# Kernel optimization log

Measured on AMD Instinct MI355X. Metric: run time of the kernel, lower is better.

## Reference

```python
import jax, jax.numpy as jnp
import numpy as np

B, L, D, H = 4, 1024, 1024, 16
HD = D // H            # head dim 64
MAXP = 1024            # max_position_embeddings
NADJ = 2               # teacher layers mapped to this student layer


def setup_inputs() -> dict:
    key = jax.random.key(0)
    ks = jax.random.split(key, 6)
    return {
        "hidden_states": jax.random.normal(ks[0], (B, L, D), jnp.float32),
        "attention_mask": jnp.zeros((B, 1, 1, L), jnp.float32),
        "teacher_w": jax.random.normal(ks[1], (3, NADJ, D, D), jnp.float32) * 0.02,
        "wl_w": jax.random.normal(ks[2], (3, NADJ), jnp.float32),
        "scale_w": jnp.ones((3, D, D), jnp.float32),
        "shift_w": jnp.zeros((3, D, D), jnp.float32),
        "teacher_b": jax.random.normal(ks[3], (3, NADJ, D), jnp.float32) * 0.02,
        "wl_b": jax.random.normal(ks[4], (3, NADJ), jnp.float32),
        "scale_b": jnp.ones((3, D), jnp.float32),
        "shift_b": jnp.zeros((3, D), jnp.float32),
        "dist_emb": jax.random.normal(ks[5], (2 * MAXP - 1, HD), jnp.float32) * 0.02,
    }


def reference(hidden_states, attention_mask, teacher_w, wl_w, scale_w, shift_w,
              teacher_b, wl_b, scale_b, shift_b, dist_emb):
    # Teacher-distilled weight/bias generation (WeightGenerator/BiasGenerator):
    # student = tanh(mode-0 contraction of teacher subset with W_l) * W + B
    w = jnp.tanh(jnp.einsum('pl,ploi->poi', wl_w, teacher_w)) * scale_w + shift_w  # [3,out,in]
    b = jnp.tanh(jnp.einsum('pl,plo->po', wl_b, teacher_b)) * scale_b + shift_b    # [3,out]

    def proj(i):
        y = jnp.einsum('bld,od->blo', hidden_states, w[i]) + b[i]
        return y.reshape(B, L, H, HD).transpose(0, 2, 1, 3)  # [B,H,L,HD]

    q, k, v = proj(0), proj(1), proj(2)

    scores = jnp.einsum('bhld,bhrd->bhlr', q, k)  # [B,H,L,L]

    # relative_key_query positional bias
    dist = jnp.arange(L)[:, None] - jnp.arange(L)[None, :] + (MAXP - 1)  # [L,L]
    pe = dist_emb[dist]                                                  # [L,L,HD]
    scores = scores \
        + jnp.einsum('bhld,lrd->bhlr', q, pe) \
        + jnp.einsum('bhrd,lrd->bhlr', k, pe)

    scores = scores / np.sqrt(HD).astype(np.float32) + attention_mask
    probs = jax.nn.softmax(scores, axis=-1)  # dropout p=0.0 (eval)

    ctx = jnp.einsum('bhlr,bhrd->bhld', probs, v)
    return ctx.transpose(0, 2, 1, 3).reshape(B, L, D)
```

## Files before the change

### kernel.cpp

```cpp
#include <hip/hip_runtime.h>
#include <hip/hip_bf16.h>
#include <math.h>

#define D_  1024
#define L_  1024
#define B_  4
#define H_  16
#define HD_ 64

typedef __attribute__((ext_vector_type(4))) short short4_t;
typedef __attribute__((ext_vector_type(8))) short short8_t;
typedef __attribute__((ext_vector_type(4))) float f4;
typedef unsigned short u16;

__device__ __forceinline__ f4 MF(short8_t a, short8_t b, f4 c) {
  return __builtin_amdgcn_mfma_f32_16x16x32_bf16(a, b, c, 0, 0, 0);
}
__device__ __forceinline__ unsigned fbits(float x) { return __builtin_bit_cast(unsigned, x); }
__device__ __forceinline__ float bf2f(unsigned short u) {
  return __builtin_bit_cast(float, (unsigned)u << 16);
}
__device__ __forceinline__ unsigned pack2hi(float x, float y) {
  return (fbits(x) >> 16) | (fbits(y) & 0xFFFF0000u);
}
__device__ __forceinline__ float bfres(float x) {
  return x - __builtin_bit_cast(float, fbits(x) & 0xFFFF0000u);
}
__device__ __forceinline__ float ftanh(float x) {
  float t = __expf(2.f * x);
  return (t - 1.f) / (t + 1.f);
}
__device__ __forceinline__ void gload16(const void* g, void* l) {
  __builtin_amdgcn_global_load_lds(
      (const __attribute__((address_space(1))) unsigned*)g,
      (__attribute__((address_space(3))) unsigned*)l, 16, 0, 0);
}
__device__ __forceinline__ short8_t ldsfragP(const char* base, int row, int ci) {
  return *(const short8_t*)(base + row * 128 + ((ci ^ (row & 7)) << 4));
}
__device__ __forceinline__ int perm32(int c) {
  return (c & ~31) | (((c >> 2) & 3) << 3) | (((c >> 4) & 1) << 2);
}

__global__ __launch_bounds__(256) void wgen_kernel(
    const float* __restrict__ tw, const float* __restrict__ wl,
    const float* __restrict__ sc, const float* __restrict__ sh,
    u16* __restrict__ whi, u16* __restrict__ wlo) {
  size_t i4 = (size_t)blockIdx.x * 256 + threadIdx.x;
  size_t e = i4 * 4;
  int p = (int)(e >> 20);
  size_t rem = e & 0xFFFFFu;
  float a0 = wl[p * 2 + 0], a1 = wl[p * 2 + 1];
  float4 t0 = *(const float4*)&tw[((size_t)(p * 2 + 0) << 20) + rem];
  float4 t1 = *(const float4*)&tw[((size_t)(p * 2 + 1) << 20) + rem];
  float4 s4 = *(const float4*)&sc[e];
  float4 h4 = *(const float4*)&sh[e];
  float4 o;
  o.x = ftanh(a0 * t0.x + a1 * t1.x) * s4.x + h4.x;
  o.y = ftanh(a0 * t0.y + a1 * t1.y) * s4.y + h4.y;
  o.z = ftanh(a0 * t0.z + a1 * t1.z) * s4.z + h4.z;
  o.w = ftanh(a0 * t0.w + a1 * t1.w) * s4.w + h4.w;
  const size_t off = (e & ~(size_t)31) + perm32((int)(e & 31));
  uint2 hi; hi.x = pack2hi(o.x, o.y); hi.y = pack2hi(o.z, o.w);
  *(uint2*)&whi[off] = hi;
  uint2 lo; lo.x = pack2hi(bfres(o.x), bfres(o.y)); lo.y = pack2hi(bfres(o.z), bfres(o.w));
  *(uint2*)&wlo[off] = lo;
}

__global__ __launch_bounds__(256) void hscvt_kernel(
    const float* __restrict__ hs,
    u16* __restrict__ hhi, u16* __restrict__ hlo) {
  size_t i4 = (size_t)blockIdx.x * 256 + threadIdx.x;
  size_t e = i4 * 4;
  float4 v = *(const float4*)&hs[e];
  const size_t off = (e & ~(size_t)31) + perm32((int)(e & 31));
  uint2 hi; hi.x = pack2hi(v.x, v.y); hi.y = pack2hi(v.z, v.w);
  *(uint2*)&hhi[off] = hi;
  uint2 lo; lo.x = pack2hi(bfres(v.x), bfres(v.y)); lo.y = pack2hi(bfres(v.z), bfres(v.w));
  *(uint2*)&hlo[off] = lo;
}

__global__ __launch_bounds__(256) void bgen_kernel(
    const float* __restrict__ tb, const float* __restrict__ wl,
    const float* __restrict__ sc, const float* __restrict__ sh,
    float* __restrict__ b_out) {
  int i = blockIdx.x * 256 + threadIdx.x;
  int p = i >> 10;
  int o = i & 1023;
  float v = ftanh(wl[p * 2 + 0] * tb[(p * 2 + 0) * D_ + o] +
                  wl[p * 2 + 1] * tb[(p * 2 + 1) * D_ + o]);
  b_out[i] = v * sc[i] + sh[i];
}

__global__ __launch_bounds__(256) void ecvt_kernel(
    const float* __restrict__ emb, u16* __restrict__ embh) {
  int i4 = blockIdx.x * 256 + threadIdx.x;
  if (i4 >= 32752) return;
  int e = i4 * 4;
  float4 v = *(const float4*)&emb[e];
  uint2 h2; h2.x = pack2hi(v.x, v.y); h2.y = pack2hi(v.z, v.w);
  int pe = (e & ~31) | perm32(e & 31);
  *(uint2*)&embh[pe] = h2;
}

__global__ __launch_bounds__(256) void proj_mfma_kernel(
    const u16* __restrict__ Ahp, const u16* __restrict__ Alp,
    const u16* __restrict__ Bhp, const u16* __restrict__ Blp,
    const float* __restrict__ bias,
    u16* __restrict__ Qhi, u16* __restrict__ Qlo,
    u16* __restrict__ Khi, u16* __restrict__ Klo,
    u16* __restrict__ Vthi, u16* __restrict__ Vtlo) {
  __shared__ u16 Ah[128][32], Al[128][32], Bh[128][32], Bl[128][32];
  const int tid  = threadIdx.x;
  const int lane = tid & 63;
  const int wv   = tid >> 6;
  const int wm   = wv >> 1, wn = wv & 1;
  const int l15  = lane & 15, g = lane >> 4;

  const int bid = (blockIdx.x & 7) * 96 + (blockIdx.x >> 3);
  const int mt = bid & 31, nt = bid >> 5;
  const int m0 = mt * 128, n0 = nt * 128;

  f4 acc[4][4];
#pragma unroll
  for (int i = 0; i < 4; ++i)
#pragma unroll
    for (int j = 0; j < 4; ++j) acc[i][j] = f4{0.f, 0.f, 0.f, 0.f};

  const int srow = lane >> 2;
  const int sck  = (lane & 3) * 8;

#pragma unroll 1
  for (int k0 = 0; k0 < D_; k0 += 32) {
#pragma unroll
    for (int s = 0; s < 8; ++s) {
      const int q = wv * 8 + s;
      const int mat   = q >> 4;
      const int plane = (q >> 3) & 1;
      const int rowg  = q & 7;
      const u16* base = mat ? (plane ? Alp : Ahp) : (plane ? Blp : Bhp);
      const int  rb   = mat ? m0 : n0;
      const u16* src = base + (size_t)(rb + rowg * 16 + srow) * 1024 + k0 + sck;
      u16* dst = (mat ? (plane ? &Al[0][0] : &Ah[0][0])
                      : (plane ? &Bl[0][0] : &Bh[0][0])) + rowg * 512;
      gload16(src, dst);
    }
    __syncthreads();

    short8_t ah[4], al[4], bh[4], bl[4];
#pragma unroll
    for (int i = 0; i < 4; ++i) {
      ah[i] = *(const short8_t*)&Ah[wm * 64 + i * 16 + l15][g * 8];
      al[i] = *(const short8_t*)&Al[wm * 64 + i * 16 + l15][g * 8];
      bh[i] = *(const short8_t*)&Bh[wn * 64 + i * 16 + l15][g * 8];
      bl[i] = *(const short8_t*)&Bl[wn * 64 + i * 16 + l15][g * 8];
    }
#pragma unroll
    for (int mi = 0; mi < 4; ++mi)
#pragma unroll
      for (int ni = 0; ni < 4; ++ni) {
        acc[mi][ni] = MF(ah[mi], bh[ni], acc[mi][ni]);
        acc[mi][ni] = MF(ah[mi], bl[ni], acc[mi][ni]);
        acc[mi][ni] = MF(al[mi], bh[ni], acc[mi][ni]);
      }
    __syncthreads();
  }

  const int p = n0 >> 10;
  const int h0 = (n0 >> 6) & 15;
  const int nbase = n0 + wn * 64;
  float bnv[4];
#pragma unroll
  for (int ni = 0; ni < 4; ++ni) bnv[ni] = bias[nbase + ni * 16 + l15];
  float* T = (float*)&Ah[0][0];

#pragma unroll
  for (int mi = 0; mi < 4; ++mi) {
    __syncthreads();
#pragma unroll
    for (int ni = 0; ni < 4; ++ni)
#pragma unroll
      for (int r = 0; r < 4; ++r)
        T[(wm * 16 + 4 * g + r) * 132 + wn * 64 + ni * 16 + l15] =
            acc[mi][ni][r] + bnv[ni];
    __syncthreads();

    if (p < 2) {
      u16* PH = p ? Khi : Qhi;
      u16* PL = p ? Klo : Qlo;
      const int lr = tid >> 3;
      const int m = m0 + (lr >> 4) * 64 + mi * 16 + (lr & 15);
      const int bb = m >> 10, l = m & 1023;
#pragma unroll
      for (int c = 0; c < 4; ++c) {
        const int col = 4 * (tid & 7) + 32 * c;
        const int pc = perm32(col & 63) | (col & 64);
        const int hd = pc & 63, hl = col >> 6;
        float4 v = *(const float4*)&T[lr * 132 + col];
        uint2 hi; hi.x = pack2hi(v.x, v.y); hi.y = pack2hi(v.z, v.w);
        uint2 lo; lo.x = pack2hi(bfres(v.x), bfres(v.y)); lo.y = pack2hi(bfres(v.z), bfres(v.w));
        const size_t ad = ((size_t)(bb * 16 + h0 + hl) << 16) + (size_t)l * 64 + hd;
        *(uint2*)&PH[ad] = hi;
        *(uint2*)&PL[ad] = lo;
      }
    } else {
      const int col = (tid >> 3) & 31;
#pragma unroll
      for (int c = 0; c < 4; ++c) {
        const int cc = col + 32 * c;
        const int hd = cc & 63, hl = cc >> 6;
        const int mq = tid & 7;
        const int lr0 = 4 * mq;
        float vv[4];
#pragma unroll
        for (int k = 0; k < 4; ++k) vv[k] = T[(lr0 + k) * 132 + cc];
        const int m = m0 + (lr0 >> 4) * 64 + mi * 16 + (lr0 & 15);
        const int bb = m >> 10, l = m & 1023;
        const int pl = (l & ~31) | perm32(l & 31);
        uint2 hi; hi.x = pack2hi(vv[0], vv[1]); hi.y = pack2hi(vv[2], vv[3]);
        uint2 lo; lo.x = pack2hi(bfres(vv[0]), bfres(vv[1]));
        lo.y = pack2hi(bfres(vv[2]), bfres(vv[3]));
        const size_t ad = ((size_t)(bb * 16 + h0 + hl) << 16) + (size_t)hd * 1024 + pl;
        *(uint2*)&Vthi[ad] = hi;
        *(uint2*)&Vtlo[ad] = lo;
      }
    }
  }
}

#define KD_OFF 0
#define VD_OFF 32768
#define ER_OFF 49152
#define UB_OFF 81920
#define WB_OFF 115712
#define SM4_SIZE 149504

__global__ __launch_bounds__(512, 2) void attn7_kernel(
    const u16* __restrict__ Qhi, const u16* __restrict__ Qlo,
    const u16* __restrict__ Khi, const u16* __restrict__ Klo,
    const u16* __restrict__ Vthi, const u16* __restrict__ Vtlo,
    const u16* __restrict__ embh, const float* __restrict__ mask,
    float* __restrict__ out) {
  __shared__ __align__(16) char sm[SM4_SIZE];
  char* ERb = sm + ER_OFF;

  const int tid  = threadIdx.x;
  const int lane = tid & 63;
  const int wv   = tid >> 6;
  const int t    = wv >> 2;
  const int lh   = (wv >> 1) & 1;
  const int rh   = wv & 1;
  const int l15  = lane & 15;
  const int g    = lane >> 4;
  const int rsub = lane >> 3;
  const int scol = ((lane & 7) ^ (lane >> 3)) << 3;

  const int bid = (blockIdx.x & 7) * 64 + (blockIdx.x >> 3);
  const int lp = bid & 7, h = (bid >> 3) & 15, b = bid >> 7;
  const int l0 = lp * 128;
  const size_t bhoff = (size_t)(b * 16 + h) << 16;
  const float* maskp = mask + b * L_;

  u16* UBt = (u16*)(sm + UB_OFF) + t * 8448;
  u16* WBt = (u16*)(sm + WB_OFF) + t * 8448;

#pragma unroll
  for (int s = 0; s < 4; ++s) {
    const int idx = wv * 4 + s;
    const int plane = idx >> 4, rowg = idx & 15;
    const u16* src = (plane ? Qlo : Qhi) + bhoff +
                     (size_t)(l0 + rowg * 8 + rsub) * 64 + scol;
    gload16(src, ERb + (plane * 16 + rowg) * 1024);
  }
  __syncthreads();

  short8_t qfh[2][2], qfl[2][2];
#pragma unroll
  for (int nb = 0; nb < 2; ++nb)
#pragma unroll
    for (int kc = 0; kc < 2; ++kc) {
      const int row = 64 * t + 32 * lh + 16 * nb + l15;
      qfh[nb][kc] = ldsfragP(ERb,         row, 4 * kc + g);
      qfl[nb][kc] = ldsfragP(ERb + 16384, row, 4 * kc + g);
    }
  __syncthreads();

  const int pl0 = (wv * 2 + 0) >> 3, rg0 = (wv * 2 + 0) & 7;
  const int pl1 = (wv * 2 + 1) >> 3, rg1 = (wv * 2 + 1) & 7;
  const u16* kb0 = (pl0 ? Klo : Khi) + bhoff + (size_t)(rg0 * 8 + rsub) * 64 + scol;
  const u16* kb1 = (pl1 ? Klo : Khi) + bhoff + (size_t)(rg1 * 8 + rsub) * 64 + scol;
  const u16* vp0 = (pl0 ? Vtlo : Vthi) + bhoff + (size_t)(rg0 * 8 + rsub) * 1024 + scol;
  const u16* vp1 = (pl1 ? Vtlo : Vthi) + bhoff + (size_t)(rg1 * 8 + rsub) * 1024 + scol;
  const u16* ep  = embh + (size_t)(l0 + 896 + wv * 8 + rsub) * 64 + scol;
  const u16* kp0 = kb0 + 4096;
  const u16* kp1 = kb1 + 4096;
  char* const kdst0 = sm + KD_OFF + pl0 * 8192 + rg0 * 1024;
  char* const kdst1 = sm + KD_OFF + pl1 * 8192 + rg1 * 1024;
  char* const vdst0 = sm + VD_OFF + pl0 * 8192 + rg0 * 1024;
  char* const vdst1 = sm + VD_OFF + pl1 * 8192 + rg1 * 1024;

  {
    gload16(kb0, kdst0);
    gload16(kb1, kdst1);
    const int dmin0 = l0 + 960;
#pragma unroll
    for (int s = 0; s < 3; ++s) {
      const int grp = wv * 3 + s;
      const int slot = (dmin0 + grp * 8) & 255;
      gload16(embh + (size_t)(dmin0 + grp * 8 + rsub) * 64 + scol,
              ERb + slot * 128);
    }
  }

  f4 o_acc[4][2];
#pragma unroll
  for (int i = 0; i < 4; ++i)
#pragma unroll
    for (int j = 0; j < 2; ++j) o_acc[i][j] = f4{0.f, 0.f, 0.f, 0.f};
  float mrun[2] = {-3e38f, -3e38f};
  float lsum[2] = {0.f, 0.f};

#pragma unroll 2
  for (int rt = 0; rt < 16; ++rt) {
    const int r0 = rt * 64;
    const int cur = rt & 1;
    const int dmin = l0 - r0 + 960;

    __syncthreads();

    if (rt < 15) {
      char* kdn = sm + KD_OFF + (cur ^ 1) * 16384;
      gload16(kp0, kdn + pl0 * 8192 + rg0 * 1024);
      gload16(kp1, kdn + pl1 * 8192 + rg1 * 1024);
      kp0 += 4096; kp1 += 4096;
      const int slot = (dmin - 64 + wv * 8) & 255;
      gload16(ep, ERb + slot * 128);
      ep -= 4096;
    }
    gload16(vp0, vdst0);
    gload16(vp1, vdst1);
    vp0 += 64; vp1 += 64;

    float4 mk[2];
#pragma unroll
    for (int mb = 0; mb < 2; ++mb)
      mk[mb] = *(const float4*)&maskp[r0 + 32 * rh + 16 * mb + 4 * g];

    const char* kdc_h = sm + KD_OFF + cur * 16384;
    const char* kdc_l = kdc_h + 8192;

    f4 sacc[2][2];
#pragma unroll
    for (int i = 0; i < 2; ++i)
#pragma unroll
      for (int j = 0; j < 2; ++j) sacc[i][j] = f4{0.f, 0.f, 0.f, 0.f};
    short8_t khf[2][2];
    __builtin_amdgcn_s_setprio(1);
#pragma unroll
    for (int mb = 0; mb < 2; ++mb)
#pragma unroll
      for (int kc = 0; kc < 2; ++kc) {
        const int row = 32 * rh + 16 * mb + l15;
        short8_t ka = ldsfragP(kdc_h, row, 4 * kc + g);
        short8_t kl = ldsfragP(kdc_l, row, 4 * kc + g);
        khf[mb][kc] = ka;
#pragma unroll
        for (int nb = 0; nb < 2; ++nb) {
          sacc[mb][nb] = MF(ka, qfh[nb][kc], sacc[mb][nb]);
          sacc[mb][nb] = MF(ka, qfl[nb][kc], sacc[mb][nb]);
          sacc[mb][nb] = MF(kl, qfh[nb][kc], sacc[mb][nb]);
        }
      }
    __builtin_amdgcn_s_setprio(0);

#pragma unroll
    for (int s = 0; s < 3; ++s) {
      const int dblk = 16 * (2 * lh + 3 * rh + s);
      const int erow = (dmin + 64 * t + dblk + l15) & 255;
      const short8_t eb0 = ldsfragP(ERb, erow, g);
      const short8_t eb1 = ldsfragP(ERb, erow, 4 + g);
      f4 au0 = f4{0.f, 0.f, 0.f, 0.f}, au1 = f4{0.f, 0.f, 0.f, 0.f};
      au0 = MF(eb0, qfh[0][0], au0); au0 = MF(eb1, qfh[0][1], au0);
      au1 = MF(eb0, qfh[1][0], au1); au1 = MF(eb1, qfh[1][1], au1);
#pragma unroll
      for (int nb = 0; nb < 2; ++nb) {
        const f4 au = nb ? au1 : au0;
        uint2 w2; w2.x = pack2hi(au[0], au[1]); w2.y = pack2hi(au[2], au[3]);
        *(uint2*)&UBt[(32 * lh + 16 * nb + l15) * 132 + dblk + 4 * g] = w2;
      }
    }

#pragma unroll
    for (int s = 0; s < 3; ++s) {
      const int dblk = 16 * ((2 - 2 * rh) + 3 * lh + s);
      const int erow = (dmin + 64 * t + dblk + l15) & 255;
      const short8_t eb0 = ldsfragP(ERb, erow, g);
      const short8_t eb1 = ldsfragP(ERb, erow, 4 + g);
      f4 aw0 = f4{0.f, 0.f, 0.f, 0.f}, aw1 = f4{0.f, 0.f, 0.f, 0.f};
      aw0 = MF(eb0, khf[0][0], aw0); aw0 = MF(eb1, khf[0][1], aw0);
      aw1 = MF(eb0, khf[1][0], aw1); aw1 = MF(eb1, khf[1][1], aw1);
#pragma unroll
      for (int mb = 0; mb < 2; ++mb) {
        const f4 aw = mb ? aw1 : aw0;
        uint2 w2; w2.x = pack2hi(aw[0], aw[1]); w2.y = pack2hi(aw[2], aw[3]);
        *(uint2*)&WBt[(32 * rh + 16 * mb + l15) * 132 + dblk + 4 * g] = w2;
      }
    }
    __syncthreads();

    float pbuf[2][2][4];
#pragma unroll
    for (int nb = 0; nb < 2; ++nb) {
      const int lA = 32 * lh + 16 * nb + l15;
      float sv[2][4];
      float ml = -3e38f;
#pragma unroll
      for (int mb = 0; mb < 2; ++mb) {
        const int rr = 32 * rh + 16 * mb + 4 * g;
        const int dbase = lA + 63 - rr;
        const float mka[4] = {mk[mb].x, mk[mb].y, mk[mb].z, mk[mb].w};
#pragma unroll
        for (int j = 0; j < 4; ++j) {
          const float uu = bf2f(UBt[lA * 132 + dbase - j]);
          const float ww = bf2f(WBt[(rr + j) * 132 + dbase - j]);
          float s = (sacc[mb][nb][j] + uu + ww) * 0.125f + mka[j];
          sv[mb][j] = s;
          ml = fmaxf(ml, s);
        }
      }
      ml = fmaxf(ml, __shfl_xor(ml, 16));
      ml = fmaxf(ml, __shfl_xor(ml, 32));
      const bool nore = __all(ml <= mrun[nb]);
      const float mn = nore ? mrun[nb] : fmaxf(mrun[nb], ml);
      float ps = 0.f;
#pragma unroll
      for (int mb = 0; mb < 2; ++mb)
#pragma unroll
        for (int j = 0; j < 4; ++j) {
          const float pv = __expf(sv[mb][j] - mn);
          pbuf[nb][mb][j] = pv;
          ps += pv;
        }
      ps += __shfl_xor(ps, 16);
      ps += __shfl_xor(ps, 32);
      if (nore) {
        lsum[nb] += ps;
      } else {
        const float rs = __expf(mrun[nb] - mn);
        lsum[nb] = lsum[nb] * rs + ps;
        mrun[nb] = mn;
#pragma unroll
        for (int mbd = 0; mbd < 4; ++mbd) {
          o_acc[mbd][nb][0] *= rs; o_acc[mbd][nb][1] *= rs;
          o_acc[mbd][nb][2] *= rs; o_acc[mbd][nb][3] *= rs;
        }
      }
    }

    short8_t pf[2], pl_[2];
#pragma unroll
    for (int nb = 0; nb < 2; ++nb) {
      union { unsigned u[4]; short8_t v; } uh, ul;
      uh.u[0] = pack2hi(pbuf[nb][0][0], pbuf[nb][0][1]);
      uh.u[1] = pack2hi(pbuf[nb][0][2], pbuf[nb][0][3]);
      uh.u[2] = pack2hi(pbuf[nb][1][0], pbuf[nb][1][1]);
      uh.u[3] = pack2hi(pbuf[nb][1][2], pbuf[nb][1][3]);
      pf[nb] = uh.v;
      ul.u[0] = pack2hi(bfres(pbuf[nb][0][0]), bfres(pbuf[nb][0][1]));
      ul.u[1] = pack2hi(bfres(pbuf[nb][0][2]), bfres(pbuf[nb][0][3]));
      ul.u[2] = pack2hi(bfres(pbuf[nb][1][0]), bfres(pbuf[nb][1][1]));
      ul.u[3] = pack2hi(bfres(pbuf[nb][1][2]), bfres(pbuf[nb][1][3]));
      pl_[nb] = ul.v;
    }
    const char* vdc_h = sm + VD_OFF;
    const char* vdc_l = vdc_h + 8192;
    __builtin_amdgcn_s_setprio(1);
#pragma unroll
    for (int mbd = 0; mbd < 4; ++mbd) {
      short8_t vh = ldsfragP(vdc_h, 16 * mbd + l15, 4 * rh + g);
      short8_t vl = ldsfragP(vdc_l, 16 * mbd + l15, 4 * rh + g);
#pragma unroll
      for (int nb = 0; nb < 2; ++nb) {
        o_acc[mbd][nb] = MF(vh, pf[nb], o_acc[mbd][nb]);
        o_acc[mbd][nb] = MF(vh, pl_[nb], o_acc[mbd][nb]);
        o_acc[mbd][nb] = MF(vl, pf[nb], o_acc[mbd][nb]);
      }
    }
    __builtin_amdgcn_s_setprio(0);
  }

  __syncthreads();
  float* mbuf = (float*)ERb;
  float* obuf = (float*)(sm + UB_OFF);
  if (g == 0) {
#pragma unroll
    for (int nb = 0; nb < 2; ++nb) {
      mbuf[((wv * 2 + nb) * 16 + l15) * 2 + 0] = mrun[nb];
      mbuf[((wv * 2 + nb) * 16 + l15) * 2 + 1] = lsum[nb];
    }
  }
  __syncthreads();
  const int pw = wv ^ 1;
  float alpha[2], ltot[2];
#pragma unroll
  for (int nb = 0; nb < 2; ++nb) {
    float m2 = mbuf[((pw * 2 + nb) * 16 + l15) * 2 + 0];
    float s2 = mbuf[((pw * 2 + nb) * 16 + l15) * 2 + 1];
    float M = fmaxf(mrun[nb], m2);
    alpha[nb] = __expf(mrun[nb] - M);
    ltot[nb] = lsum[nb] * alpha[nb] + s2 * __expf(m2 - M);
  }
  const int pair = wv >> 1;
  if (rh == 1) {
#pragma unroll
    for (int mbd = 0; mbd < 4; ++mbd)
#pragma unroll
      for (int nb = 0; nb < 2; ++nb)
#pragma unroll
        for (int j = 0; j < 4; ++j)
          obuf[(pair * 64 + 16 * mbd + 4 * g + j) * 32 + 16 * nb + l15] =
              o_acc[mbd][nb][j] * alpha[nb];
  }
  __syncthreads();
  if (rh == 0) {
#pragma unroll
    for (int mbd = 0; mbd < 4; ++mbd)
#pragma unroll
      for (int nb = 0; nb < 2; ++nb) {
        const int lgl = l0 + 64 * t + 32 * lh + 16 * nb + l15;
        const float inv = 1.f / ltot[nb];
        float tmp[4];
#pragma unroll
        for (int j = 0; j < 4; ++j)
          tmp[j] = (o_acc[mbd][nb][j] * alpha[nb] +
                    obuf[(pair * 64 + 16 * mbd + 4 * g + j) * 32 + 16 * nb + l15]) * inv;
        float4 ov; ov.x = tmp[0]; ov.y = tmp[1]; ov.z = tmp[2]; ov.w = tmp[3];
        *(float4*)&out[(size_t)(b * L_ + lgl) * D_ + h * HD_ + 16 * mbd + 4 * g] = ov;
      }
  }
}

extern "C" void kernel_launch(void* const* d_in, const int* in_sizes, int n_in,
                              void* d_out, int out_size, void* d_ws, size_t ws_size,
                              hipStream_t stream) {
  const float* hs   = (const float*)d_in[0];
  const float* mask = (const float*)d_in[1];
  const float* tw   = (const float*)d_in[2];
  const float* wlw  = (const float*)d_in[3];
  const float* scw  = (const float*)d_in[4];
  const float* shw  = (const float*)d_in[5];
  const float* tb   = (const float*)d_in[6];
  const float* wlb  = (const float*)d_in[7];
  const float* scb  = (const float*)d_in[8];
  const float* shb  = (const float*)d_in[9];
  const float* emb  = (const float*)d_in[10];
  float* out = (float*)d_out;

  char* W = (char*)d_ws;
  float* b_s = (float*)W;
  u16* whi  = (u16*)(W + 12288);
  u16* wlo  = whi + 3145728;
  u16* embh = wlo + 3145728;
  u16* Qhi  = embh + 131072;
  u16* Qlo  = Qhi + 4194304;
  u16* Khi  = Qlo + 4194304;
  u16* Klo  = Khi + 4194304;
  u16* Vthi = Klo + 4194304;
  u16* Vtlo = Vthi + 4194304;
  u16* hhi  = Vtlo + 4194304;
  u16* hlo  = hhi + 4194304;

  hipLaunchKernelGGL(wgen_kernel, dim3(3072), dim3(256), 0, stream,
                     tw, wlw, scw, shw, whi, wlo);
  hipLaunchKernelGGL(hscvt_kernel, dim3(4096), dim3(256), 0, stream,
                     hs, hhi, hlo);
  hipLaunchKernelGGL(bgen_kernel, dim3(12), dim3(256), 0, stream,
                     tb, wlb, scb, shb, b_s);
  hipLaunchKernelGGL(ecvt_kernel, dim3(128), dim3(256), 0, stream, emb, embh);
  hipLaunchKernelGGL(proj_mfma_kernel, dim3(768), dim3(256), 0, stream,
                     hhi, hlo, whi, wlo, b_s, Qhi, Qlo, Khi, Klo, Vthi, Vtlo);
  hipLaunchKernelGGL(attn7_kernel, dim3(512), dim3(512), 0, stream,
                     Qhi, Qlo, Khi, Klo, Vthi, Vtlo, embh, mask, out);
}
```

Before: 251.1 us.

## Fuse prep kernels into one launch and double-buffer projection GEMM loads

The four elementwise preparation kernels (weight generation, hidden-state split, embedding convert, bias generation) are merged into a single launch whose block ranges dispatch to each task. This removes three kernel launches and the gaps between them. The projection GEMM now double-buffers its LDS tiles: it prefetches the next k-slice while computing the current one, needs one barrier per iteration instead of two, and raises wave priority around the MFMA block. In exchange, LDS use doubles and a launch-bounds hint of 2 blocks per CU is added, which may constrain registers.

After: 231.1 us. 8.0% less time.

```diff
diff --git a/kernel.cpp b/kernel.cpp
--- a/kernel.cpp
+++ b/kernel.cpp
@@ -42,75 +42,73 @@
   return (c & ~31) | (((c >> 2) & 3) << 3) | (((c >> 4) & 1) << 2);
 }
 
-__global__ __launch_bounds__(256) void wgen_kernel(
-    const float* __restrict__ tw, const float* __restrict__ wl,
-    const float* __restrict__ sc, const float* __restrict__ sh,
-    u16* __restrict__ whi, u16* __restrict__ wlo) {
-  size_t i4 = (size_t)blockIdx.x * 256 + threadIdx.x;
-  size_t e = i4 * 4;
-  int p = (int)(e >> 20);
-  size_t rem = e & 0xFFFFFu;
-  float a0 = wl[p * 2 + 0], a1 = wl[p * 2 + 1];
-  float4 t0 = *(const float4*)&tw[((size_t)(p * 2 + 0) << 20) + rem];
-  float4 t1 = *(const float4*)&tw[((size_t)(p * 2 + 1) << 20) + rem];
-  float4 s4 = *(const float4*)&sc[e];
-  float4 h4 = *(const float4*)&sh[e];
-  float4 o;
-  o.x = ftanh(a0 * t0.x + a1 * t1.x) * s4.x + h4.x;
-  o.y = ftanh(a0 * t0.y + a1 * t1.y) * s4.y + h4.y;
-  o.z = ftanh(a0 * t0.z + a1 * t1.z) * s4.z + h4.z;
-  o.w = ftanh(a0 * t0.w + a1 * t1.w) * s4.w + h4.w;
-  const size_t off = (e & ~(size_t)31) + perm32((int)(e & 31));
-  uint2 hi; hi.x = pack2hi(o.x, o.y); hi.y = pack2hi(o.z, o.w);
-  *(uint2*)&whi[off] = hi;
-  uint2 lo; lo.x = pack2hi(bfres(o.x), bfres(o.y)); lo.y = pack2hi(bfres(o.z), bfres(o.w));
-  *(uint2*)&wlo[off] = lo;
-}
-
-__global__ __launch_bounds__(256) void hscvt_kernel(
+__global__ __launch_bounds__(256) void prep_kernel(
+    const float* __restrict__ tw, const float* __restrict__ wlw,
+    const float* __restrict__ scw, const float* __restrict__ shw,
     const float* __restrict__ hs,
-    u16* __restrict__ hhi, u16* __restrict__ hlo) {
-  size_t i4 = (size_t)blockIdx.x * 256 + threadIdx.x;
-  size_t e = i4 * 4;
-  float4 v = *(const float4*)&hs[e];
-  const size_t off = (e & ~(size_t)31) + perm32((int)(e & 31));
-  uint2 hi; hi.x = pack2hi(v.x, v.y); hi.y = pack2hi(v.z, v.w);
-  *(uint2*)&hhi[off] = hi;
-  uint2 lo; lo.x = pack2hi(bfres(v.x), bfres(v.y)); lo.y = pack2hi(bfres(v.z), bfres(v.w));
-  *(uint2*)&hlo[off] = lo;
-}
-
-__global__ __launch_bounds__(256) void bgen_kernel(
-    const float* __restrict__ tb, const float* __restrict__ wl,
-    const float* __restrict__ sc, const float* __restrict__ sh,
-    float* __restrict__ b_out) {
-  int i = blockIdx.x * 256 + threadIdx.x;
-  int p = i >> 10;
-  int o = i & 1023;
-  float v = ftanh(wl[p * 2 + 0] * tb[(p * 2 + 0) * D_ + o] +
-                  wl[p * 2 + 1] * tb[(p * 2 + 1) * D_ + o]);
-  b_out[i] = v * sc[i] + sh[i];
-}
-
-__global__ __launch_bounds__(256) void ecvt_kernel(
-    const float* __restrict__ emb, u16* __restrict__ embh) {
-  int i4 = blockIdx.x * 256 + threadIdx.x;
-  if (i4 >= 32752) return;
-  int e = i4 * 4;
-  float4 v = *(const float4*)&emb[e];
-  uint2 h2; h2.x = pack2hi(v.x, v.y); h2.y = pack2hi(v.z, v.w);
-  int pe = (e & ~31) | perm32(e & 31);
-  *(uint2*)&embh[pe] = h2;
-}
-
-__global__ __launch_bounds__(256) void proj_mfma_kernel(
+    const float* __restrict__ tb, const float* __restrict__ wlb,
+    const float* __restrict__ scb, const float* __restrict__ shb,
+    const float* __restrict__ emb,
+    u16* __restrict__ whi, u16* __restrict__ wlo,
+    u16* __restrict__ hhi, u16* __restrict__ hlo,
+    u16* __restrict__ embh, float* __restrict__ b_s) {
+  const int blk = blockIdx.x;
+  const int tid = threadIdx.x;
+  if (blk < 3072) {
+    size_t i4 = (size_t)blk * 256 + tid;
+    size_t e = i4 * 4;
+    int p = (int)(e >> 20);
+    size_t rem = e & 0xFFFFFu;
+    float a0 = wlw[p * 2 + 0], a1 = wlw[p * 2 + 1];
+    float4 t0 = *(const float4*)&tw[((size_t)(p * 2 + 0) << 20) + rem];
+    float4 t1 = *(const float4*)&tw[((size_t)(p * 2 + 1) << 20) + rem];
+    float4 s4 = *(const float4*)&scw[e];
+    float4 h4 = *(const float4*)&shw[e];
+    float4 o;
+    o.x = ftanh(a0 * t0.x + a1 * t1.x) * s4.x + h4.x;
+    o.y = ftanh(a0 * t0.y + a1 * t1.y) * s4.y + h4.y;
+    o.z = ftanh(a0 * t0.z + a1 * t1.z) * s4.z + h4.z;
+    o.w = ftanh(a0 * t0.w + a1 * t1.w) * s4.w + h4.w;
+    const size_t off = (e & ~(size_t)31) + perm32((int)(e & 31));
+    uint2 hi; hi.x = pack2hi(o.x, o.y); hi.y = pack2hi(o.z, o.w);
+    *(uint2*)&whi[off] = hi;
+    uint2 lo; lo.x = pack2hi(bfres(o.x), bfres(o.y)); lo.y = pack2hi(bfres(o.z), bfres(o.w));
+    *(uint2*)&wlo[off] = lo;
+  } else if (blk < 7168) {
+    size_t i4 = (size_t)(blk - 3072) * 256 + tid;
+    size_t e = i4 * 4;
+    float4 v = *(const float4*)&hs[e];
+    const size_t off = (e & ~(size_t)31) + perm32((int)(e & 31));
+    uint2 hi; hi.x = pack2hi(v.x, v.y); hi.y = pack2hi(v.z, v.w);
+    *(uint2*)&hhi[off] = hi;
+    uint2 lo; lo.x = pack2hi(bfres(v.x), bfres(v.y)); lo.y = pack2hi(bfres(v.z), bfres(v.w));
+    *(uint2*)&hlo[off] = lo;
+  } else if (blk < 7296) {
+    int i4 = (blk - 7168) * 256 + tid;
+    if (i4 >= 32752) return;
+    int e = i4 * 4;
+    float4 v = *(const float4*)&emb[e];
+    uint2 h2; h2.x = pack2hi(v.x, v.y); h2.y = pack2hi(v.z, v.w);
+    int pe = (e & ~31) | perm32(e & 31);
+    *(uint2*)&embh[pe] = h2;
+  } else {
+    int i = (blk - 7296) * 256 + tid;
+    int p = i >> 10;
+    int o = i & 1023;
+    float v = ftanh(wlb[p * 2 + 0] * tb[(p * 2 + 0) * D_ + o] +
+                    wlb[p * 2 + 1] * tb[(p * 2 + 1) * D_ + o]);
+    b_s[i] = v * scb[i] + shb[i];
+  }
+}
+
+__global__ __launch_bounds__(256, 2) void proj_mfma_kernel(
     const u16* __restrict__ Ahp, const u16* __restrict__ Alp,
     const u16* __restrict__ Bhp, const u16* __restrict__ Blp,
     const float* __restrict__ bias,
     u16* __restrict__ Qhi, u16* __restrict__ Qlo,
     u16* __restrict__ Khi, u16* __restrict__ Klo,
     u16* __restrict__ Vthi, u16* __restrict__ Vtlo) {
-  __shared__ u16 Ah[128][32], Al[128][32], Bh[128][32], Bl[128][32];
+  __shared__ u16 SB[2][4][128][32];
   const int tid  = threadIdx.x;
   const int lane = tid & 63;
   const int wv   = tid >> 6;
@@ -130,31 +128,45 @@
   const int srow = lane >> 2;
   const int sck  = (lane & 3) * 8;
 
-#pragma unroll 1
-  for (int k0 = 0; k0 < D_; k0 += 32) {
-#pragma unroll
-    for (int s = 0; s < 8; ++s) {
-      const int q = wv * 8 + s;
-      const int mat   = q >> 4;
-      const int plane = (q >> 3) & 1;
-      const int rowg  = q & 7;
-      const u16* base = mat ? (plane ? Alp : Ahp) : (plane ? Blp : Bhp);
-      const int  rb   = mat ? m0 : n0;
-      const u16* src = base + (size_t)(rb + rowg * 16 + srow) * 1024 + k0 + sck;
-      u16* dst = (mat ? (plane ? &Al[0][0] : &Ah[0][0])
-                      : (plane ? &Bl[0][0] : &Bh[0][0])) + rowg * 512;
-      gload16(src, dst);
-    }
+  const u16* sbase[8];
+  u16* sdst[8];
+#pragma unroll
+  for (int s = 0; s < 8; ++s) {
+    const int q = wv * 8 + s;
+    const int mat   = q >> 4;
+    const int plane = (q >> 3) & 1;
+    const int rowg  = q & 7;
+    const u16* base = mat ? (plane ? Alp : Ahp) : (plane ? Blp : Bhp);
+    const int  rb   = mat ? m0 : n0;
+    sbase[s] = base + (size_t)(rb + rowg * 16 + srow) * 1024 + sck;
+    sdst[s]  = &SB[0][(mat ^ 1) * 2 + plane][rowg * 16][0];
+  }
+
+#pragma unroll
+  for (int s = 0; s < 8; ++s) gload16(sbase[s], sdst[s]);
+
+#pragma unroll 2
+  for (int kt = 0; kt < 32; ++kt) {
+    const int cur = kt & 1;
     __syncthreads();
 
+    if (kt < 31) {
+      const int k1 = (kt + 1) * 32;
+      const int bo = (cur ^ 1) * 16384;
+#pragma unroll
+      for (int s = 0; s < 8; ++s) gload16(sbase[s] + k1, sdst[s] + bo);
+    }
+
+    const u16 (*SBc)[128][32] = SB[cur];
     short8_t ah[4], al[4], bh[4], bl[4];
 #pragma unroll
     for (int i = 0; i < 4; ++i) {
-      ah[i] = *(const short8_t*)&Ah[wm * 64 + i * 16 + l15][g * 8];
-      al[i] = *(const short8_t*)&Al[wm * 64 + i * 16 + l15][g * 8];
-      bh[i] = *(const short8_t*)&Bh[wn * 64 + i * 16 + l15][g * 8];
-      bl[i] = *(const short8_t*)&Bl[wn * 64 + i * 16 + l15][g * 8];
-    }
+      ah[i] = *(const short8_t*)&SBc[0][wm * 64 + i * 16 + l15][g * 8];
+      al[i] = *(const short8_t*)&SBc[1][wm * 64 + i * 16 + l15][g * 8];
+      bh[i] = *(const short8_t*)&SBc[2][wn * 64 + i * 16 + l15][g * 8];
+      bl[i] = *(const short8_t*)&SBc[3][wn * 64 + i * 16 + l15][g * 8];
+    }
+    __builtin_amdgcn_s_setprio(1);
 #pragma unroll
     for (int mi = 0; mi < 4; ++mi)
 #pragma unroll
@@ -163,7 +175,7 @@
         acc[mi][ni] = MF(ah[mi], bl[ni], acc[mi][ni]);
         acc[mi][ni] = MF(al[mi], bh[ni], acc[mi][ni]);
       }
-    __syncthreads();
+    __builtin_amdgcn_s_setprio(0);
   }
 
   const int p = n0 >> 10;
@@ -172,7 +184,7 @@
   float bnv[4];
 #pragma unroll
   for (int ni = 0; ni < 4; ++ni) bnv[ni] = bias[nbase + ni * 16 + l15];
-  float* T = (float*)&Ah[0][0];
+  float* T = (float*)&SB[0][0][0][0];
 
 #pragma unroll
   for (int mi = 0; mi < 4; ++mi) {
@@ -570,13 +582,9 @@
   u16* hhi  = Vtlo + 4194304;
   u16* hlo  = hhi + 4194304;
 
-  hipLaunchKernelGGL(wgen_kernel, dim3(3072), dim3(256), 0, stream,
-                     tw, wlw, scw, shw, whi, wlo);
-  hipLaunchKernelGGL(hscvt_kernel, dim3(4096), dim3(256), 0, stream,
-                     hs, hhi, hlo);
-  hipLaunchKernelGGL(bgen_kernel, dim3(12), dim3(256), 0, stream,
-                     tb, wlb, scb, shb, b_s);
-  hipLaunchKernelGGL(ecvt_kernel, dim3(128), dim3(256), 0, stream, emb, embh);
+  hipLaunchKernelGGL(prep_kernel, dim3(7308), dim3(256), 0, stream,
+                     tw, wlw, scw, shw, hs, tb, wlb, scb, shb, emb,
+                     whi, wlo, hhi, hlo, embh, b_s);
   hipLaunchKernelGGL(proj_mfma_kernel, dim3(768), dim3(256), 0, stream,
                      hhi, hlo, whi, wlo, b_s, Qhi, Qlo, Khi, Klo, Vthi, Vtlo);
   hipLaunchKernelGGL(attn7_kernel, dim3(512), dim3(512), 0, stream,
```
